# Kernel optimization log

Hardware: AMD Instinct MI355X
Metric: run time of the kernel (lower is better)

## Reference

```python
import jax, jax.numpy as jnp
import numpy as np

E = 1024   # embedding_dim
H = 16     # num_head
D = 64     # dim_head (E == H*D)
R = 8      # LoRA rank
BATCH = 2
SEQ = 2048
EPS = 1e-6


def setup_inputs() -> dict:
    key = jax.random.key(0)
    ks = jax.random.split(key, 16)
    s = 0.02
    return {
        "y": jax.random.normal(ks[0], (BATCH, SEQ, E), jnp.float32),
        "Wqkv": jax.random.normal(ks[1], (3 * E, E), jnp.float32) * s,
        "bqkv": jax.random.normal(ks[2], (3 * E,), jnp.float32) * s,
        "Wmsa": jax.random.normal(ks[3], (E, E), jnp.float32) * s,
        "Bq": jax.random.normal(ks[4], (E, R), jnp.float32) * s,
        "Aq": jax.random.normal(ks[5], (R, E), jnp.float32) * s,
        "Bk": jax.random.normal(ks[6], (E, R), jnp.float32) * s,
        "Ak": jax.random.normal(ks[7], (R, E), jnp.float32) * s,
        "Bv": jax.random.normal(ks[8], (E, R), jnp.float32) * s,
        "Av": jax.random.normal(ks[9], (R, E), jnp.float32) * s,
        "Bo": jax.random.normal(ks[10], (E, R), jnp.float32) * s,
        "Ao": jax.random.normal(ks[11], (R, E), jnp.float32) * s,
        "gamma": jnp.ones((E,), jnp.float32),
        "beta": jnp.zeros((E,), jnp.float32),
        "i": 0,
    }


def reference(y, Wqkv, bqkv, Wmsa, Bq, Aq, Bk, Ak, Bv, Av, Bo, Ao, gamma, beta, i):
    B, S, En = y.shape
    # fused QKV projection: nn.Linear -> y @ W.T + b
    qkv = (y @ Wqkv.T + bqkv).reshape(B, S, 3, H, D).transpose(2, 0, 3, 1, 4)
    Q, K, V = qkv[0], qkv[1], qkv[2]          # each [B,H,S,D]

    def lora_delta(Bw, Aw):
        # torch: y @ (B.weight @ A.weight), reshaped to heads
        return (y @ (Bw @ Aw)).reshape(B, S, H, D).transpose(0, 2, 1, 3)

    Q = Q + lora_delta(Bq, Aq)
    K = K + lora_delta(Bk, Ak)
    V = V + lora_delta(Bv, Av)

    scale = jnp.asarray(np.sqrt(D), y.dtype)
    scores = jnp.einsum('bhqd,bhkd->bhqk', Q, K) / scale
    attn = jax.nn.softmax(scores, axis=-1)
    o = jnp.einsum('bhqk,bhkd->bhqd', attn, V)          # [B,H,S,D]
    o = o.transpose(0, 2, 1, 3).reshape(B, S, H * D)    # [B,S,E]

    msa = o @ Wmsa.T + o @ (Bo @ Ao)
    res = msa + y

    mu = jnp.mean(res, axis=-1, keepdims=True)
    var = jnp.var(res, axis=-1, keepdims=True)
    return (res - mu) * jax.lax.rsqrt(var + EPS) * gamma + beta
```

## Files before the change

### kernel.cpp

```cpp
#include <hip/hip_runtime.h>
#include <hip/hip_bf16.h>
#include <stdint.h>

typedef __attribute__((ext_vector_type(8))) short short8;
typedef __attribute__((ext_vector_type(4))) float f32x4;

typedef const __attribute__((address_space(1))) void gv_t;
typedef __attribute__((address_space(3))) void lv_t;

__device__ __forceinline__ void gl_lds16(const void* g, void* l) {
    __builtin_amdgcn_global_load_lds((gv_t*)g, (lv_t*)l, 16, 0, 0);
}

__device__ __forceinline__ unsigned short f2bf(float f) {
    union { float f; unsigned int u; } v; v.f = f;
    unsigned int r = v.u + 0x7fffu + ((v.u >> 16) & 1u);
    return (unsigned short)(r >> 16);
}

__device__ __forceinline__ unsigned int pack2bf(float a, float b) {
    union { __hip_bfloat162 h2; unsigned int u; } cv;
    cv.h2 = __float22bfloat162_rn(make_float2(a, b));
    return cv.u;
}

__device__ __forceinline__ f32x4 zero4() { f32x4 z = {0.f, 0.f, 0.f, 0.f}; return z; }

__global__ void k_cvt(const float* __restrict__ y, unsigned short* __restrict__ yb) {
    int i = (blockIdx.x * 256 + threadIdx.x) * 4;
    float4 v = *(const float4*)(y + i);
    union { unsigned short u[4]; uint2 w; } o;
    o.u[0] = f2bf(v.x); o.u[1] = f2bf(v.y); o.u[2] = f2bf(v.z); o.u[3] = f2bf(v.w);
    *(uint2*)(yb + i) = o.w;
}

__global__ void k_wqkv(const float* __restrict__ W,
                       const float* __restrict__ Bq, const float* __restrict__ Aq,
                       const float* __restrict__ Bk, const float* __restrict__ Ak,
                       const float* __restrict__ Bv, const float* __restrict__ Av,
                       unsigned short* __restrict__ out) {
    int idx = blockIdx.x * 256 + threadIdx.x;
    int n = idx >> 10, k = idx & 1023;
    int sel = n >> 10, n0 = n & 1023;
    const float* Bp = (sel == 0) ? Bq : (sel == 1) ? Bk : Bv;
    const float* Ap = (sel == 0) ? Aq : (sel == 1) ? Ak : Av;
    float acc = W[idx];
    #pragma unroll
    for (int r = 0; r < 8; ++r) acc += Bp[k * 8 + r] * Ap[r * 1024 + n0];
    out[idx] = f2bf(acc);
}

__global__ void k_wmsa(const float* __restrict__ W,
                       const float* __restrict__ Bo, const float* __restrict__ Ao,
                       unsigned short* __restrict__ out) {
    int idx = blockIdx.x * 256 + threadIdx.x;
    int n = idx >> 10, k = idx & 1023;
    float acc = W[idx];
    #pragma unroll
    for (int r = 0; r < 8; ++r) acc += Bo[k * 8 + r] * Ao[r * 1024 + n];
    out[idx] = f2bf(acc);
}

template <int EPI>
__global__ __launch_bounds__(256, 2) void k_gemm(const unsigned short* __restrict__ Ag,
                                                 const unsigned short* __restrict__ Bg,
                                                 const float* __restrict__ bias,
                                                 const float* __restrict__ yres,
                                                 void* __restrict__ Cout,
                                                 int M, int N, int K) {
    __shared__ unsigned short As[128 * 32];
    __shared__ unsigned short Bs[128 * 32];
    const int flat = threadIdx.x;
    const int m0 = blockIdx.y * 128, n0 = blockIdx.x * 128;
    const int lane = flat & 63, wave = flat >> 6;
    const int l16 = lane & 15, quad = lane >> 4;
    const int wm = (wave >> 1) * 64, wn = (wave & 1) * 64;

    f32x4 acc[4][4];
    #pragma unroll
    for (int mi = 0; mi < 4; ++mi)
        #pragma unroll
        for (int ni = 0; ni < 4; ++ni) acc[mi][ni] = zero4();

    const unsigned short* ap = Ag + (size_t)(m0 + (flat >> 2)) * K + (flat & 3) * 8;
    const unsigned short* bp = Bg + (size_t)(n0 + (flat >> 2)) * K + (flat & 3) * 8;
    const size_t rstep = (size_t)64 * K;

    for (int k0 = 0; k0 < K; k0 += 32) {
        __syncthreads();
        gl_lds16(ap,         &As[flat * 8]);
        gl_lds16(ap + rstep, &As[2048 + flat * 8]);
        gl_lds16(bp,         &Bs[flat * 8]);
        gl_lds16(bp + rstep, &Bs[2048 + flat * 8]);
        ap += 32; bp += 32;
        __syncthreads();

        short8 af[4], bfr[4];
        #pragma unroll
        for (int i = 0; i < 4; ++i) af[i] = *(const short8*)&As[(wm + i * 16 + l16) * 32 + quad * 8];
        #pragma unroll
        for (int i = 0; i < 4; ++i) bfr[i] = *(const short8*)&Bs[(wn + i * 16 + l16) * 32 + quad * 8];
        #pragma unroll
        for (int mi = 0; mi < 4; ++mi)
            #pragma unroll
            for (int ni = 0; ni < 4; ++ni)
                acc[mi][ni] = __builtin_amdgcn_mfma_f32_16x16x32_bf16(af[mi], bfr[ni], acc[mi][ni], 0, 0, 0);
    }

    if (EPI == 0) {
        unsigned short* C = (unsigned short*)Cout;
        #pragma unroll
        for (int ni = 0; ni < 4; ++ni) {
            int col = n0 + wn + ni * 16 + l16;
            float bv = bias[col];
            #pragma unroll
            for (int mi = 0; mi < 4; ++mi) {
                int row = m0 + wm + mi * 16 + quad * 4;
                #pragma unroll
                for (int r = 0; r < 4; ++r)
                    C[(size_t)(row + r) * N + col] = f2bf(acc[mi][ni][r] + bv);
            }
        }
    } else {
        float* C = (float*)Cout;
        #pragma unroll
        for (int ni = 0; ni < 4; ++ni) {
            int col = n0 + wn + ni * 16 + l16;
            #pragma unroll
            for (int mi = 0; mi < 4; ++mi) {
                int row = m0 + wm + mi * 16 + quad * 4;
                #pragma unroll
                for (int r = 0; r < 4; ++r)
                    C[(size_t)(row + r) * N + col] = acc[mi][ni][r] + yres[(size_t)(row + r) * N + col];
            }
        }
    }
}

__global__ __launch_bounds__(256) void k_vt(const unsigned short* __restrict__ qkv,
                                            unsigned short* __restrict__ vtg) {
    __shared__ unsigned short T[64 * 72];
    const int t = threadIdx.x;
    const int k0 = blockIdx.x * 64, h = blockIdx.y, b = blockIdx.z;
    const unsigned short* vbase = qkv + (size_t)(b * 2048) * 3072 + 2048 + h * 64;
    #pragma unroll
    for (int i = 0; i < 2; ++i) {
        int B = i * 256 + t;
        int row = B >> 3, c = B & 7;
        short8 v = *(const short8*)(vbase + (size_t)(k0 + row) * 3072 + c * 8);
        *(short8*)&T[row * 72 + c * 8] = v;
    }
    __syncthreads();
    unsigned short* obase = vtg + ((size_t)((b * 16 + h) * 64)) * 2048 + k0;
    #pragma unroll
    for (int i = 0; i < 2; ++i) {
        int B = i * 256 + t;
        int d = B >> 3, kc = B & 7;
        union { unsigned short u[8]; short8 v; } pk;
        #pragma unroll
        for (int jj = 0; jj < 8; ++jj) pk.u[jj] = T[(kc * 8 + jj) * 72 + d];
        *(short8*)(obase + (size_t)d * 2048 + kc * 8) = pk.v;
    }
}

__global__ __launch_bounds__(256, 2) void k_attn(const unsigned short* __restrict__ qkv,
                                                 const unsigned short* __restrict__ vtg,
                                                 unsigned short* __restrict__ o) {
    __shared__ unsigned short LDS[24576];
    unsigned short* Qs = LDS;
    unsigned short* Ps = LDS;
    unsigned short* Ks0 = LDS + 8192;
    unsigned short* Vt0 = LDS + 16384;

    const int t = threadIdx.x;
    const int lane = t & 63, wave = t >> 6;
    const int l16 = lane & 15, quad = lane >> 4;
    const int l8 = l16 & 7;
    const int q0 = blockIdx.x * 128;
    const int h = blockIdx.y, b = blockIdx.z;

    const unsigned short* qbase = qkv + (size_t)(b * 2048) * 3072 + h * 64;
    const unsigned short* kbase = qbase + 1024;
    const unsigned short* vtbase = vtg + (size_t)((b * 16 + h) * 64) * 2048;

    #pragma unroll
    for (int i = 0; i < 4; ++i) {
        int B = i * 256 + t;
        int row = B >> 3, c = (B & 7) ^ (row & 7);
        gl_lds16(qbase + (size_t)(q0 + row) * 3072 + c * 8, &Qs[B * 8]);
    }

    const int B0 = t, B1 = t + 256;
    const int r0 = B0 >> 3, c0 = (B0 & 7) ^ (r0 & 7);
    const int r1 = B1 >> 3, c1 = (B1 & 7) ^ (r1 & 7);
    const unsigned short* kp0 = kbase + (size_t)r0 * 3072 + c0 * 8;
    const unsigned short* kp1 = kbase + (size_t)r1 * 3072 + c1 * 8;
    const unsigned short* vp0 = vtbase + (size_t)r0 * 2048 + c0 * 8;
    const unsigned short* vp1 = vtbase + (size_t)r1 * 2048 + c1 * 8;

    gl_lds16(kp0, &Ks0[B0 * 8]);
    gl_lds16(kp1, &Ks0[B1 * 8]);
    gl_lds16(vp0, &Vt0[B0 * 8]);
    gl_lds16(vp1, &Vt0[B1 * 8]);
    kp0 += 64 * 3072; kp1 += 64 * 3072; vp0 += 64; vp1 += 64;

    __syncthreads();

    short8 qf[2][2];
    #pragma unroll
    for (int ni = 0; ni < 2; ++ni)
        #pragma unroll
        for (int kk = 0; kk < 2; ++kk)
            qf[ni][kk] = *(const short8*)&Qs[(wave * 32 + ni * 16 + l16) * 64 + ((kk * 4 + quad) ^ l8) * 8];

    __syncthreads();

    f32x4 acc_o[2][4];
    #pragma unroll
    for (int mo = 0; mo < 2; ++mo)
        #pragma unroll
        for (int nd = 0; nd < 4; ++nd) acc_o[mo][nd] = zero4();
    float lsum[2] = {0.f, 0.f};
    const float SC  = 0.18033688011112042f;
    const float MST = 8.0f;

    for (int j = 0; j < 32; ++j) {
        const unsigned short* Ks = Ks0 + (j & 1) * 4096;
        const unsigned short* Vt = Vt0 + (j & 1) * 4096;

        if (j < 31) {
            unsigned short* Kn = Ks0 + ((j + 1) & 1) * 4096;
            unsigned short* Vn = Vt0 + ((j + 1) & 1) * 4096;
            gl_lds16(kp0, &Kn[B0 * 8]);
            gl_lds16(kp1, &Kn[B1 * 8]);
            gl_lds16(vp0, &Vn[B0 * 8]);
            gl_lds16(vp1, &Vn[B1 * 8]);
            kp0 += 64 * 3072; kp1 += 64 * 3072; vp0 += 64; vp1 += 64;
        }

        f32x4 sacc[4][2];
        #pragma unroll
        for (int mi = 0; mi < 4; ++mi)
            #pragma unroll
            for (int ni = 0; ni < 2; ++ni) sacc[mi][ni] = zero4();
        #pragma unroll
        for (int kk = 0; kk < 2; ++kk)
            #pragma unroll
            for (int mi = 0; mi < 4; ++mi) {
                short8 kf = *(const short8*)&Ks[(mi * 16 + l16) * 64 + ((kk * 4 + quad) ^ l8) * 8];
                #pragma unroll
                for (int ni = 0; ni < 2; ++ni)
                    sacc[mi][ni] = __builtin_amdgcn_mfma_f32_16x16x32_bf16(kf, qf[ni][kk], sacc[mi][ni], 0, 0, 0);
            }

        #pragma unroll
        for (int ni = 0; ni < 2; ++ni) {
            int qrow = wave * 32 + ni * 16 + l16;
            #pragma unroll
            for (int mi = 0; mi < 4; ++mi) {
                float p0 = exp2f(__builtin_fmaf(sacc[mi][ni][0], SC, -MST));
                float p1 = exp2f(__builtin_fmaf(sacc[mi][ni][1], SC, -MST));
                float p2 = exp2f(__builtin_fmaf(sacc[mi][ni][2], SC, -MST));
                float p3 = exp2f(__builtin_fmaf(sacc[mi][ni][3], SC, -MST));
                lsum[ni] += (p0 + p1) + (p2 + p3);
                uint2 w; w.x = pack2bf(p0, p1); w.y = pack2bf(p2, p3);
                *(uint2*)&Ps[qrow * 64 + ((2 * mi + (quad >> 1)) ^ l8) * 8 + (quad & 1) * 4] = w;
            }
        }

        #pragma unroll
        for (int kk = 0; kk < 2; ++kk) {
            short8 pf[2];
            #pragma unroll
            for (int mo = 0; mo < 2; ++mo)
                pf[mo] = *(const short8*)&Ps[(wave * 32 + mo * 16 + l16) * 64 + ((kk * 4 + quad) ^ l8) * 8];
            #pragma unroll
            for (int nd = 0; nd < 4; ++nd) {
                short8 vf = *(const short8*)&Vt[(nd * 16 + l16) * 64 + ((kk * 4 + quad) ^ l8) * 8];
                #pragma unroll
                for (int mo = 0; mo < 2; ++mo)
                    acc_o[mo][nd] = __builtin_amdgcn_mfma_f32_16x16x32_bf16(pf[mo], vf, acc_o[mo][nd], 0, 0, 0);
            }
        }

        __syncthreads();
    }

    #pragma unroll
    for (int ni = 0; ni < 2; ++ni) {
        lsum[ni] += __shfl_xor(lsum[ni], 16);
        lsum[ni] += __shfl_xor(lsum[ni], 32);
    }
    #pragma unroll
    for (int mo = 0; mo < 2; ++mo)
        #pragma unroll
        for (int rr = 0; rr < 4; ++rr) {
            float lr = __shfl(lsum[mo], quad * 4 + rr, 16);
            float inv = 1.f / lr;
            int qg = q0 + wave * 32 + mo * 16 + quad * 4 + rr;
            size_t base = ((size_t)(b * 2048 + qg)) * 1024 + h * 64;
            #pragma unroll
            for (int nd = 0; nd < 4; ++nd)
                o[base + nd * 16 + l16] = f2bf(acc_o[mo][nd][rr] * inv);
        }
}

__global__ __launch_bounds__(256) void k_ln(const float* __restrict__ res,
                                            const float* __restrict__ g,
                                            const float* __restrict__ be,
                                            float* __restrict__ out) {
    __shared__ float red[8];
    const int row = blockIdx.x, t = threadIdx.x;
    const float* x = res + (size_t)row * 1024;
    float4 v = *(const float4*)(x + t * 4);
    float s = v.x + v.y + v.z + v.w;
    float sq = v.x * v.x + v.y * v.y + v.z * v.z + v.w * v.w;
    #pragma unroll
    for (int off = 32; off; off >>= 1) { s += __shfl_down(s, off); sq += __shfl_down(sq, off); }
    if ((t & 63) == 0) { red[t >> 6] = s; red[4 + (t >> 6)] = sq; }
    __syncthreads();
    float ts = red[0] + red[1] + red[2] + red[3];
    float tq = red[4] + red[5] + red[6] + red[7];
    float mu = ts * (1.f / 1024.f);
    float var = tq * (1.f / 1024.f) - mu * mu;
    float rstd = rsqrtf(var + 1e-6f);
    float4 gg = *(const float4*)(g + t * 4);
    float4 bb = *(const float4*)(be + t * 4);
    float4 ov;
    ov.x = (v.x - mu) * rstd * gg.x + bb.x;
    ov.y = (v.y - mu) * rstd * gg.y + bb.y;
    ov.z = (v.z - mu) * rstd * gg.z + bb.z;
    ov.w = (v.w - mu) * rstd * gg.w + bb.w;
    *(float4*)(out + (size_t)row * 1024 + t * 4) = ov;
}

extern "C" void kernel_launch(void* const* d_in, const int* in_sizes, int n_in,
                              void* d_out, int out_size, void* d_ws, size_t ws_size,
                              hipStream_t stream) {
    (void)in_sizes; (void)n_in; (void)out_size; (void)ws_size;
    const float* y    = (const float*)d_in[0];
    const float* Wqkv = (const float*)d_in[1];
    const float* bqkv = (const float*)d_in[2];
    const float* Wmsa = (const float*)d_in[3];
    const float* Bq = (const float*)d_in[4];
    const float* Aq = (const float*)d_in[5];
    const float* Bk = (const float*)d_in[6];
    const float* Ak = (const float*)d_in[7];
    const float* Bv = (const float*)d_in[8];
    const float* Av = (const float*)d_in[9];
    const float* Bo = (const float*)d_in[10];
    const float* Ao = (const float*)d_in[11];
    const float* gamma = (const float*)d_in[12];
    const float* beta  = (const float*)d_in[13];

    char* ws = (char*)d_ws;
    unsigned short* yb   = (unsigned short*)(ws);
    unsigned short* weq  = (unsigned short*)(ws + (8u  << 20));
    unsigned short* wem  = (unsigned short*)(ws + (14u << 20));
    unsigned short* qkv  = (unsigned short*)(ws + (16u << 20));
    unsigned short* vtg  = (unsigned short*)(ws + (40u << 20));
    unsigned short* obuf = yb;
    float* res = (float*)qkv;

    k_cvt <<<4096, 256, 0, stream>>>(y, yb);
    k_wqkv<<<12288, 256, 0, stream>>>(Wqkv, Bq, Aq, Bk, Ak, Bv, Av, weq);
    k_wmsa<<<4096, 256, 0, stream>>>(Wmsa, Bo, Ao, wem);
    k_gemm<0><<<dim3(24, 32), 256, 0, stream>>>(yb, weq, bqkv, nullptr, (void*)qkv, 4096, 3072, 1024);
    k_vt  <<<dim3(32, 16, 2), 256, 0, stream>>>(qkv, vtg);
    k_attn<<<dim3(16, 16, 2), 256, 0, stream>>>(qkv, vtg, obuf);
    k_gemm<1><<<dim3(8, 32), 256, 0, stream>>>(obuf, wem, nullptr, y, (void*)res, 4096, 1024, 1024);
    k_ln  <<<4096, 256, 0, stream>>>(res, gamma, beta, (float*)d_out);
}
```

Measured before the change: 258.9 us.

## Double-buffer GEMM LDS tiles, shrink output GEMM tile, fold softmax scale into Q

The GEMM kernel now prefetches the next K-slice into a second LDS buffer while computing on the current one, removing one barrier per iteration. The output projection GEMM is templated to 64-row tiles, launching twice as many blocks to improve CU occupancy. The softmax scale times log2(e) is folded into the Q weights and bias, so the attention inner loop calls exp2 directly without an FMA and without the constant max-shift. Dropping the shift relies on scores staying small enough to avoid overflow in exp2.

```diff
diff --git a/kernel.cpp b/kernel.cpp
--- a/kernel.cpp
+++ b/kernel.cpp
@@ -7,6 +7,8 @@
 
 typedef const __attribute__((address_space(1))) void gv_t;
 typedef __attribute__((address_space(3))) void lv_t;
+
+#define SCQ 0.18033688011112042f
 
 __device__ __forceinline__ void gl_lds16(const void* g, void* l) {
     __builtin_amdgcn_global_load_lds((gv_t*)g, (lv_t*)l, 16, 0, 0);
@@ -47,7 +49,7 @@
     float acc = W[idx];
     #pragma unroll
     for (int r = 0; r < 8; ++r) acc += Bp[k * 8 + r] * Ap[r * 1024 + n0];
-    out[idx] = f2bf(acc);
+    out[idx] = f2bf(acc * ((sel == 0) ? SCQ : 1.0f));
 }
 
 __global__ void k_wmsa(const float* __restrict__ W,
@@ -61,58 +63,73 @@
     out[idx] = f2bf(acc);
 }
 
-template <int EPI>
+template <int TM, int EPI>
 __global__ __launch_bounds__(256, 2) void k_gemm(const unsigned short* __restrict__ Ag,
                                                  const unsigned short* __restrict__ Bg,
                                                  const float* __restrict__ bias,
                                                  const float* __restrict__ yres,
                                                  void* __restrict__ Cout,
                                                  int M, int N, int K) {
-    __shared__ unsigned short As[128 * 32];
-    __shared__ unsigned short Bs[128 * 32];
+    constexpr int WAVES_N = 256 / TM;
+    constexpr int WN = TM / 2;
+    constexpr int NI = WN / 16;
+    constexpr int ACALLS = TM / 64;
+    __shared__ unsigned short As[2][TM * 32];
+    __shared__ unsigned short Bs[2][128 * 32];
     const int flat = threadIdx.x;
-    const int m0 = blockIdx.y * 128, n0 = blockIdx.x * 128;
+    const int m0 = blockIdx.y * TM, n0 = blockIdx.x * 128;
     const int lane = flat & 63, wave = flat >> 6;
     const int l16 = lane & 15, quad = lane >> 4;
-    const int wm = (wave >> 1) * 64, wn = (wave & 1) * 64;
-
-    f32x4 acc[4][4];
+    const int wm = (wave / WAVES_N) * 64, wn = (wave % WAVES_N) * WN;
+
+    f32x4 acc[4][NI];
     #pragma unroll
     for (int mi = 0; mi < 4; ++mi)
         #pragma unroll
-        for (int ni = 0; ni < 4; ++ni) acc[mi][ni] = zero4();
+        for (int ni = 0; ni < NI; ++ni) acc[mi][ni] = zero4();
 
     const unsigned short* ap = Ag + (size_t)(m0 + (flat >> 2)) * K + (flat & 3) * 8;
     const unsigned short* bp = Bg + (size_t)(n0 + (flat >> 2)) * K + (flat & 3) * 8;
     const size_t rstep = (size_t)64 * K;
 
+    #pragma unroll
+    for (int c = 0; c < ACALLS; ++c) gl_lds16(ap + c * rstep, &As[0][c * 2048 + flat * 8]);
+    gl_lds16(bp,         &Bs[0][flat * 8]);
+    gl_lds16(bp + rstep, &Bs[0][2048 + flat * 8]);
+    ap += 32; bp += 32;
+    __syncthreads();
+
     for (int k0 = 0; k0 < K; k0 += 32) {
+        const int cur = (k0 >> 5) & 1;
+        if (k0 + 32 < K) {
+            const int nxt = cur ^ 1;
+            #pragma unroll
+            for (int c = 0; c < ACALLS; ++c) gl_lds16(ap + c * rstep, &As[nxt][c * 2048 + flat * 8]);
+            gl_lds16(bp,         &Bs[nxt][flat * 8]);
+            gl_lds16(bp + rstep, &Bs[nxt][2048 + flat * 8]);
+            ap += 32; bp += 32;
+        }
+
+        short8 af[4], bfr[NI];
+        #pragma unroll
+        for (int i = 0; i < 4; ++i) af[i] = *(const short8*)&As[cur][(wm + i * 16 + l16) * 32 + quad * 8];
+        #pragma unroll
+        for (int i = 0; i < NI; ++i) bfr[i] = *(const short8*)&Bs[cur][(wn + i * 16 + l16) * 32 + quad * 8];
+        #pragma unroll
+        for (int mi = 0; mi < 4; ++mi)
+            #pragma unroll
+            for (int ni = 0; ni < NI; ++ni)
+                acc[mi][ni] = __builtin_amdgcn_mfma_f32_16x16x32_bf16(af[mi], bfr[ni], acc[mi][ni], 0, 0, 0);
+
         __syncthreads();
-        gl_lds16(ap,         &As[flat * 8]);
-        gl_lds16(ap + rstep, &As[2048 + flat * 8]);
-        gl_lds16(bp,         &Bs[flat * 8]);
-        gl_lds16(bp + rstep, &Bs[2048 + flat * 8]);
-        ap += 32; bp += 32;
-        __syncthreads();
-
-        short8 af[4], bfr[4];
-        #pragma unroll
-        for (int i = 0; i < 4; ++i) af[i] = *(const short8*)&As[(wm + i * 16 + l16) * 32 + quad * 8];
-        #pragma unroll
-        for (int i = 0; i < 4; ++i) bfr[i] = *(const short8*)&Bs[(wn + i * 16 + l16) * 32 + quad * 8];
-        #pragma unroll
-        for (int mi = 0; mi < 4; ++mi)
-            #pragma unroll
-            for (int ni = 0; ni < 4; ++ni)
-                acc[mi][ni] = __builtin_amdgcn_mfma_f32_16x16x32_bf16(af[mi], bfr[ni], acc[mi][ni], 0, 0, 0);
     }
 
     if (EPI == 0) {
         unsigned short* C = (unsigned short*)Cout;
         #pragma unroll
-        for (int ni = 0; ni < 4; ++ni) {
+        for (int ni = 0; ni < NI; ++ni) {
             int col = n0 + wn + ni * 16 + l16;
-            float bv = bias[col];
+            float bv = bias[col] * ((col < 1024) ? SCQ : 1.0f);
             #pragma unroll
             for (int mi = 0; mi < 4; ++mi) {
                 int row = m0 + wm + mi * 16 + quad * 4;
@@ -124,7 +141,7 @@
     } else {
         float* C = (float*)Cout;
         #pragma unroll
-        for (int ni = 0; ni < 4; ++ni) {
+        for (int ni = 0; ni < NI; ++ni) {
             int col = n0 + wn + ni * 16 + l16;
             #pragma unroll
             for (int mi = 0; mi < 4; ++mi) {
@@ -221,8 +238,6 @@
         #pragma unroll
         for (int nd = 0; nd < 4; ++nd) acc_o[mo][nd] = zero4();
     float lsum[2] = {0.f, 0.f};
-    const float SC  = 0.18033688011112042f;
-    const float MST = 8.0f;
 
     for (int j = 0; j < 32; ++j) {
         const unsigned short* Ks = Ks0 + (j & 1) * 4096;
@@ -258,10 +273,10 @@
             int qrow = wave * 32 + ni * 16 + l16;
             #pragma unroll
             for (int mi = 0; mi < 4; ++mi) {
-                float p0 = exp2f(__builtin_fmaf(sacc[mi][ni][0], SC, -MST));
-                float p1 = exp2f(__builtin_fmaf(sacc[mi][ni][1], SC, -MST));
-                float p2 = exp2f(__builtin_fmaf(sacc[mi][ni][2], SC, -MST));
-                float p3 = exp2f(__builtin_fmaf(sacc[mi][ni][3], SC, -MST));
+                float p0 = exp2f(sacc[mi][ni][0]);
+                float p1 = exp2f(sacc[mi][ni][1]);
+                float p2 = exp2f(sacc[mi][ni][2]);
+                float p3 = exp2f(sacc[mi][ni][3]);
                 lsum[ni] += (p0 + p1) + (p2 + p3);
                 uint2 w; w.x = pack2bf(p0, p1); w.y = pack2bf(p2, p3);
                 *(uint2*)&Ps[qrow * 64 + ((2 * mi + (quad >> 1)) ^ l8) * 8 + (quad & 1) * 4] = w;
@@ -365,9 +380,9 @@
     k_cvt <<<4096, 256, 0, stream>>>(y, yb);
     k_wqkv<<<12288, 256, 0, stream>>>(Wqkv, Bq, Aq, Bk, Ak, Bv, Av, weq);
     k_wmsa<<<4096, 256, 0, stream>>>(Wmsa, Bo, Ao, wem);
-    k_gemm<0><<<dim3(24, 32), 256, 0, stream>>>(yb, weq, bqkv, nullptr, (void*)qkv, 4096, 3072, 1024);
+    k_gemm<128, 0><<<dim3(24, 32), 256, 0, stream>>>(yb, weq, bqkv, nullptr, (void*)qkv, 4096, 3072, 1024);
     k_vt  <<<dim3(32, 16, 2), 256, 0, stream>>>(qkv, vtg);
     k_attn<<<dim3(16, 16, 2), 256, 0, stream>>>(qkv, vtg, obuf);
-    k_gemm<1><<<dim3(8, 32), 256, 0, stream>>>(obuf, wem, nullptr, y, (void*)res, 4096, 1024, 1024);
+    k_gemm<64, 1><<<dim3(8, 64), 256, 0, stream>>>(obuf, wem, nullptr, y, (void*)res, 4096, 1024, 1024);
     k_ln  <<<4096, 256, 0, stream>>>(res, gamma, beta, (float*)d_out);
 }
```

Result: faster. 241.0 us (-6.9%).
